# Kernel tuning notes

Measured on AMD Instinct MI355X. Metric: run time of the kernel, lower is better.

## Reference

```python
import jax, jax.numpy as jnp
import numpy as np


def _seg_mean(feat, dst, n):
    # mean aggregation of gathered source features onto destination nodes
    s = jax.ops.segment_sum(feat, dst, num_segments=n)
    c = jax.ops.segment_sum(jnp.ones((dst.shape[0], 1), feat.dtype), dst, num_segments=n)
    return s / jnp.maximum(c, 1.0)


def setup_inputs() -> dict:
    key = jax.random.key(0)
    ks = jax.random.split(key, 16)
    N0, N1, N2 = 400000, 100000, 25000
    E0, E1 = 1600000, 400000
    IN, HID, OUT = 128, 256, 64
    inp = {
        "x_tar": jax.random.normal(ks[0], (N0, IN), jnp.float32),
        "x_neigh": jax.random.normal(ks[1], (N0, IN), jnp.float32),
        "edge_src0": jax.random.randint(ks[2], (E0,), 0, N0, jnp.int64).astype(jnp.int32),
        "edge_dst0": jax.random.randint(ks[3], (E0,), 0, N1, jnp.int64).astype(jnp.int32),
        "edge_src1": jax.random.randint(ks[4], (E1,), 0, N1, jnp.int64).astype(jnp.int32),
        "edge_dst1": jax.random.randint(ks[5], (E1,), 0, N2, jnp.int64).astype(jnp.int32),
        "n_dst0": N1,
        "n_dst1": N2,
    }
    s = 1.0 / np.sqrt(IN)
    sh = 1.0 / np.sqrt(HID)
    inp["Wl0"] = jax.random.uniform(ks[6], (IN, HID), jnp.float32, -s, s)
    inp["Wr0"] = jax.random.uniform(ks[7], (IN, HID), jnp.float32, -s, s)
    inp["b0"] = jnp.zeros((HID,), jnp.float32)
    inp["Wl1"] = jax.random.uniform(ks[8], (HID, HID), jnp.float32, -sh, sh)
    inp["Wr1"] = jax.random.uniform(ks[9], (HID, HID), jnp.float32, -sh, sh)
    inp["b1"] = jnp.zeros((HID,), jnp.float32)
    inp["Wl2"] = jax.random.uniform(ks[10], (HID, OUT), jnp.float32, -sh, sh)
    inp["Wr2"] = jax.random.uniform(ks[11], (HID, OUT), jnp.float32, -sh, sh)
    inp["b2"] = jnp.zeros((OUT,), jnp.float32)
    return inp


def reference(x_tar, x_neigh, edge_src0, edge_dst0, edge_src1, edge_dst1,
              n_dst0, n_dst1, Wl0, Wr0, b0, Wl1, Wr1, b1, Wl2, Wr2, b2):
    # layer 0: precomputed neighbor aggregation -> lin_l(x_neigh) + lin_r(x_tar)
    x = x_neigh @ Wl0 + x_tar @ Wr0 + b0  # [N0, HID]
    # layer 1: bipartite mean-aggregate SAGEConv + relu (eval mode: dropout is identity)
    x_t = x[:n_dst0]
    aggr = _seg_mean(x[edge_src0], edge_dst0, n_dst0)
    x = jax.nn.relu(aggr @ Wl1 + x_t @ Wr1 + b1)  # [N1, HID]
    # layer 2: final SAGEConv
    x_t = x[:n_dst1]
    aggr = _seg_mean(x[edge_src1], edge_dst1, n_dst1)
    out = aggr @ Wl2 + x_t @ Wr2 + b2  # [N2, OUT]
    return jax.nn.log_softmax(out, axis=-1)
```

## Files before the change

kernel.cpp:

```cpp
#include <hip/hip_runtime.h>
#include <hip/hip_bf16.h>

typedef __bf16 bf16_t;
typedef __bf16 bf16x8_t __attribute__((ext_vector_type(8)));
typedef __bf16 bf16x4_t __attribute__((ext_vector_type(4)));
typedef float  f32x4_t  __attribute__((ext_vector_type(4)));

#define N1_ROWS 100000
#define N2_ROWS 25000
#define DIN  128
#define DHID 256
#define DOUT 64
#define CAP  96

__global__ __launch_bounds__(256) void prep_weights(
    const float* __restrict__ Wl0, const float* __restrict__ Wr0,
    const float* __restrict__ Wl1, const float* __restrict__ Wr1,
    const float* __restrict__ Wl2, const float* __restrict__ Wr2,
    bf16_t* __restrict__ Wl0T, bf16_t* __restrict__ Wr0T,
    bf16_t* __restrict__ Wl1T, bf16_t* __restrict__ Wr1T,
    bf16_t* __restrict__ Wl2T, bf16_t* __restrict__ Wr2T) {
  int b = blockIdx.x;
  const float* W; bf16_t* WT; int K, N, base;
  if      (b < 128) { W = Wl0; WT = Wl0T; K = 128; N = 256; base = 0;   }
  else if (b < 256) { W = Wr0; WT = Wr0T; K = 128; N = 256; base = 128; }
  else if (b < 512) { W = Wl1; WT = Wl1T; K = 256; N = 256; base = 256; }
  else if (b < 768) { W = Wr1; WT = Wr1T; K = 256; N = 256; base = 512; }
  else if (b < 832) { W = Wl2; WT = Wl2T; K = 256; N = 64;  base = 768; }
  else              { W = Wr2; WT = Wr2T; K = 256; N = 64;  base = 832; }
  int gid = (b - base) * 256 + threadIdx.x;
  int n = gid / K, k = gid - n * K;
  WT[gid] = (bf16_t)W[(size_t)k * N + n];
}

template<int NT, bool RELU, bool OUTF32, bool AF32>
__global__ __launch_bounds__(256) void gemm_fast(
    const void* __restrict__ A1v, const void* __restrict__ A2v,
    const bf16_t* __restrict__ W1T, const bf16_t* __restrict__ W2T,
    const float* __restrict__ bias, void* __restrict__ outp,
    int M, int K1, int K2) {
  constexpr int BK = 32;
  constexpr int LDA = 40;
  __shared__ bf16_t sA[64 * LDA];
  const int tid  = threadIdx.x;
  const int wave = tid >> 6, lane = tid & 63;
  const int l15  = lane & 15, quad = lane >> 4;
  const int rowBase = blockIdx.x * 64;
  const int colBase = wave * (NT * 16);
  constexpr int NOUT = NT * 64;

  f32x4_t acc[4][NT];
#pragma unroll
  for (int mt = 0; mt < 4; ++mt)
#pragma unroll
    for (int nt = 0; nt < NT; ++nt) acc[mt][nt] = (f32x4_t){0.f, 0.f, 0.f, 0.f};

  const int sr = tid >> 2;
  const int sc = (tid & 3) * 8;
  int gr = rowBase + sr; if (gr >= M) gr = M - 1;

  for (int half = 0; half < 2; ++half) {
    const void* A = half ? A2v : A1v;
    const bf16_t* WT = half ? W2T : W1T;
    const int K = half ? K2 : K1;
    for (int k0 = 0; k0 < K; k0 += BK) {
      bf16x8_t bf[NT];
#pragma unroll
      for (int nt = 0; nt < NT; ++nt)
        bf[nt] = *(const bf16x8_t*)&WT[(size_t)(colBase + nt * 16 + l15) * K + k0 + quad * 8];
      __syncthreads();
      if (AF32) {
        const float* Af = (const float*)A;
        float4 lo = *(const float4*)&Af[(size_t)gr * K + k0 + sc];
        float4 hi = *(const float4*)&Af[(size_t)gr * K + k0 + sc + 4];
        bf16x8_t v;
        v[0] = (bf16_t)lo.x; v[1] = (bf16_t)lo.y; v[2] = (bf16_t)lo.z; v[3] = (bf16_t)lo.w;
        v[4] = (bf16_t)hi.x; v[5] = (bf16_t)hi.y; v[6] = (bf16_t)hi.z; v[7] = (bf16_t)hi.w;
        *(bf16x8_t*)&sA[sr * LDA + sc] = v;
      } else {
        *(uint4*)&sA[sr * LDA + sc] =
            *(const uint4*)&((const bf16_t*)A)[(size_t)gr * K + k0 + sc];
      }
      __syncthreads();
#pragma unroll
      for (int mt = 0; mt < 4; ++mt) {
        bf16x8_t af = *(const bf16x8_t*)&sA[(mt * 16 + l15) * LDA + quad * 8];
#pragma unroll
        for (int nt = 0; nt < NT; ++nt)
          acc[mt][nt] = __builtin_amdgcn_mfma_f32_16x16x32_bf16(af, bf[nt], acc[mt][nt], 0, 0, 0);
      }
    }
  }

  const int rb = rowBase + quad * 4;
#pragma unroll
  for (int mt = 0; mt < 4; ++mt)
#pragma unroll
    for (int nt = 0; nt < NT; ++nt) {
      int col = colBase + nt * 16 + l15;
      float bv = bias[col];
#pragma unroll
      for (int i = 0; i < 4; ++i) {
        int row = rb + mt * 16 + i;
        if (row < M) {
          float v = acc[mt][nt][i] + bv;
          if (RELU) v = fmaxf(v, 0.f);
          if (OUTF32) ((float*)outp)[(size_t)row * NOUT + col] = v;
          else        ((bf16_t*)outp)[(size_t)row * NOUT + col] = (bf16_t)v;
        }
      }
    }
}

__global__ __launch_bounds__(256) void csr_append2(
    const int* __restrict__ s0, const int* __restrict__ d0, int E0,
    int* __restrict__ cnt0, int* __restrict__ csr0,
    const int* __restrict__ s1, const int* __restrict__ d1, int E1,
    int* __restrict__ cnt1, int* __restrict__ csr1, int B0) {
  int b = blockIdx.x;
  if (b < B0) {
    int e = b * 256 + threadIdx.x;
    if (e < E0) {
      int d = d0[e];
      int pos = atomicAdd(&cnt0[d], 1);
      if (pos < CAP) csr0[(size_t)d * CAP + pos] = s0[e];
    }
  } else {
    int e = (b - B0) * 256 + threadIdx.x;
    if (e < E1) {
      int d = d1[e];
      int pos = atomicAdd(&cnt1[d], 1);
      if (pos < CAP) csr1[(size_t)d * CAP + pos] = s1[e];
    }
  }
}

__global__ __launch_bounds__(256) void gather_mean(
    const bf16_t* __restrict__ X, const int* __restrict__ csr,
    const int* __restrict__ cnt, bf16_t* __restrict__ outp, int n) {
  int gid = blockIdx.x * 256 + threadIdx.x;
  int d = gid >> 6, lane = gid & 63;
  if (d >= n) return;
  int deg = cnt[d]; if (deg > CAP) deg = CAP;
  const int* bucket = csr + (size_t)d * CAP;
  f32x4_t A0 = {0,0,0,0}, A1 = {0,0,0,0}, A2 = {0,0,0,0}, A3 = {0,0,0,0};
  int i = 0;
  for (; i + 4 <= deg; i += 4) {
    int s0 = bucket[i], s1 = bucket[i+1], s2 = bucket[i+2], s3 = bucket[i+3];
    bf16x4_t v0 = *(const bf16x4_t*)(X + (size_t)s0 * DHID + lane * 4);
    bf16x4_t v1 = *(const bf16x4_t*)(X + (size_t)s1 * DHID + lane * 4);
    bf16x4_t v2 = *(const bf16x4_t*)(X + (size_t)s2 * DHID + lane * 4);
    bf16x4_t v3 = *(const bf16x4_t*)(X + (size_t)s3 * DHID + lane * 4);
#pragma unroll
    for (int j = 0; j < 4; ++j) {
      A0[j] += (float)v0[j]; A1[j] += (float)v1[j];
      A2[j] += (float)v2[j]; A3[j] += (float)v3[j];
    }
  }
  for (; i < deg; ++i) {
    int s = bucket[i];
    bf16x4_t v = *(const bf16x4_t*)(X + (size_t)s * DHID + lane * 4);
#pragma unroll
    for (int j = 0; j < 4; ++j) A0[j] += (float)v[j];
  }
  float inv = 1.f / (float)(deg > 0 ? deg : 1);
  bf16x4_t o;
#pragma unroll
  for (int j = 0; j < 4; ++j)
    o[j] = (bf16_t)((A0[j] + A1[j] + A2[j] + A3[j]) * inv);
  *(bf16x4_t*)(outp + (size_t)d * DHID + lane * 4) = o;
}

__global__ __launch_bounds__(256) void log_softmax64(
    float* __restrict__ logits, int R) {
  int gid = blockIdx.x * 256 + threadIdx.x;
  int row = gid >> 6, lane = gid & 63;
  if (row >= R) return;
  float v = logits[(size_t)row * DOUT + lane];
  float m = v;
  for (int o = 32; o > 0; o >>= 1) m = fmaxf(m, __shfl_xor(m, o, 64));
  float e = expf(v - m);
  float s = e;
  for (int o = 32; o > 0; o >>= 1) s += __shfl_xor(s, o, 64);
  logits[(size_t)row * DOUT + lane] = v - m - logf(s);
}

extern "C" void kernel_launch(void* const* d_in, const int* in_sizes, int n_in,
                              void* d_out, int out_size, void* d_ws, size_t ws_size,
                              hipStream_t stream) {
  const float* x_tar   = (const float*)d_in[0];
  const float* x_neigh = (const float*)d_in[1];
  const int* es0 = (const int*)d_in[2];
  const int* ed0 = (const int*)d_in[3];
  const int* es1 = (const int*)d_in[4];
  const int* ed1 = (const int*)d_in[5];
  const float* Wl0 = (const float*)d_in[8];
  const float* Wr0 = (const float*)d_in[9];
  const float* b0  = (const float*)d_in[10];
  const float* Wl1 = (const float*)d_in[11];
  const float* Wr1 = (const float*)d_in[12];
  const float* b1  = (const float*)d_in[13];
  const float* Wl2 = (const float*)d_in[14];
  const float* Wr2 = (const float*)d_in[15];
  const float* b2  = (const float*)d_in[16];

  const int E0 = in_sizes[2];
  const int E1 = in_sizes[4];
  const int M0 = in_sizes[0] / DIN;

  char* ws = (char*)d_ws;
  bf16_t* Wl0T = (bf16_t*)(ws + 0);
  bf16_t* Wr0T = (bf16_t*)(ws + 65536);
  bf16_t* Wl1T = (bf16_t*)(ws + 131072);
  bf16_t* Wr1T = (bf16_t*)(ws + 262144);
  bf16_t* Wl2T = (bf16_t*)(ws + 393216);
  bf16_t* Wr2T = (bf16_t*)(ws + 425984);
  bf16_t* x0     = (bf16_t*)(ws + 524288);
  bf16_t* x1     = (bf16_t*)(ws + 524288 + 51200000);
  bf16_t* aggrB  = (bf16_t*)(ws + 205324288);
  bf16_t* aggr2B = (bf16_t*)(ws + 256524288);
  int*    csr0   = (int*)(ws + 269324288);
  int*    csr1   = (int*)(ws + 307724288);
  int*    cnt0   = (int*)(ws + 317324288);
  int*    cnt1   = (int*)(ws + 317724288);
  float*  logits = (float*)d_out;

  prep_weights<<<896, 256, 0, stream>>>(Wl0, Wr0, Wl1, Wr1, Wl2, Wr2,
                                        Wl0T, Wr0T, Wl1T, Wr1T, Wl2T, Wr2T);

  hipMemsetAsync(cnt0, 0, (size_t)(N1_ROWS + N2_ROWS) * 4, stream);

  {
    int B0 = (E0 + 255) / 256, B1 = (E1 + 255) / 256;
    csr_append2<<<B0 + B1, 256, 0, stream>>>(es0, ed0, E0, cnt0, csr0,
                                             es1, ed1, E1, cnt1, csr1, B0);
  }

  gemm_fast<4, false, false, true><<<(M0 + 63) / 64, 256, 0, stream>>>(
      x_neigh, x_tar, Wl0T, Wr0T, b0, x0, M0, DIN, DIN);

  gather_mean<<<(int)(((long long)N1_ROWS * 64 + 255) / 256), 256, 0, stream>>>(
      x0, csr0, cnt0, aggrB, N1_ROWS);

  gemm_fast<4, true, false, false><<<(N1_ROWS + 63) / 64, 256, 0, stream>>>(
      aggrB, x0, Wl1T, Wr1T, b1, x1, N1_ROWS, DHID, DHID);

  gather_mean<<<(int)(((long long)N2_ROWS * 64 + 255) / 256), 256, 0, stream>>>(
      x1, csr1, cnt1, aggr2B, N2_ROWS);

  gemm_fast<1, false, true, false><<<(N2_ROWS + 63) / 64, 256, 0, stream>>>(
      aggr2B, x1, Wl2T, Wr2T, b2, logits, N2_ROWS, DHID, DHID);

  log_softmax64<<<(int)(((long long)N2_ROWS * 64 + 255) / 256), 256, 0, stream>>>(
      logits, N2_ROWS);
}
```

Measured before the change: 942.3 us.

## Stage full-K A tile in LDS once per GEMM half instead of per-32 chunk

The GEMM now loads the whole K extent of each 64-row A tile into shared memory in one pass. For the 128+128 layer both inputs go into one buffer; for the 256-wide layers each input is staged in its own phase. This removes the two barriers per 32-wide K step, issues all global loads up front for more memory-level parallelism, and makes K compile-time constant so loops fully unroll. In exchange LDS use grows to about 33 KB per block, which may reduce occupancy, and the loads are no longer interleaved with MFMA work.

```diff
diff --git a/kernel.cpp b/kernel.cpp
--- a/kernel.cpp
+++ b/kernel.cpp
@@ -33,14 +33,48 @@
   WT[gid] = (bf16_t)W[(size_t)k * N + n];
 }
 
-template<int NT, bool RELU, bool OUTF32, bool AF32>
+template<int KC, int LDA, bool AF32>
+__device__ __forceinline__ void stage_tile(
+    const void* __restrict__ Av, bf16_t* __restrict__ sAp,
+    int gr, int sr, int sc, int colOff) {
+  constexpr int NCH = KC / 32;
+  if (AF32) {
+    const float* Af = (const float*)Av;
+    float4 lo[NCH], hi[NCH];
+#pragma unroll
+    for (int c = 0; c < NCH; ++c) {
+      lo[c] = *(const float4*)&Af[(size_t)gr * KC + sc + c * 32];
+      hi[c] = *(const float4*)&Af[(size_t)gr * KC + sc + c * 32 + 4];
+    }
+#pragma unroll
+    for (int c = 0; c < NCH; ++c) {
+      bf16x8_t v;
+      v[0] = (bf16_t)lo[c].x; v[1] = (bf16_t)lo[c].y;
+      v[2] = (bf16_t)lo[c].z; v[3] = (bf16_t)lo[c].w;
+      v[4] = (bf16_t)hi[c].x; v[5] = (bf16_t)hi[c].y;
+      v[6] = (bf16_t)hi[c].z; v[7] = (bf16_t)hi[c].w;
+      *(bf16x8_t*)&sAp[sr * LDA + colOff + sc + c * 32] = v;
+    }
+  } else {
+    const bf16_t* Ab = (const bf16_t*)Av;
+    uint4 v[NCH];
+#pragma unroll
+    for (int c = 0; c < NCH; ++c)
+      v[c] = *(const uint4*)&Ab[(size_t)gr * KC + sc + c * 32];
+#pragma unroll
+    for (int c = 0; c < NCH; ++c)
+      *(uint4*)&sAp[sr * LDA + colOff + sc + c * 32] = v[c];
+  }
+}
+
+template<int NT, int K1, int K2, bool RELU, bool OUTF32, bool AF32>
 __global__ __launch_bounds__(256) void gemm_fast(
     const void* __restrict__ A1v, const void* __restrict__ A2v,
     const bf16_t* __restrict__ W1T, const bf16_t* __restrict__ W2T,
-    const float* __restrict__ bias, void* __restrict__ outp,
-    int M, int K1, int K2) {
-  constexpr int BK = 32;
-  constexpr int LDA = 40;
+    const float* __restrict__ bias, void* __restrict__ outp, int M) {
+  constexpr bool ONE = (K1 + K2 <= 256);
+  constexpr int KS   = ONE ? (K1 + K2) : (K1 > K2 ? K1 : K2);
+  constexpr int LDA  = KS + 8;
   __shared__ bf16_t sA[64 * LDA];
   const int tid  = threadIdx.x;
   const int wave = tid >> 6, lane = tid & 63;
@@ -59,35 +93,54 @@
   const int sc = (tid & 3) * 8;
   int gr = rowBase + sr; if (gr >= M) gr = M - 1;
 
-  for (int half = 0; half < 2; ++half) {
-    const void* A = half ? A2v : A1v;
-    const bf16_t* WT = half ? W2T : W1T;
-    const int K = half ? K2 : K1;
-    for (int k0 = 0; k0 < K; k0 += BK) {
+  if constexpr (ONE) {
+    stage_tile<K1, LDA, AF32>(A1v, sA, gr, sr, sc, 0);
+    stage_tile<K2, LDA, AF32>(A2v, sA, gr, sr, sc, K1);
+    __syncthreads();
+#pragma unroll
+    for (int ks = 0; ks < (K1 + K2) / 32; ++ks) {
+      const bool h2 = (ks * 32 >= K1);
+      const bf16_t* __restrict__ WT = h2 ? W2T : W1T;
+      const int K  = h2 ? K2 : K1;
+      const int kk = h2 ? (ks * 32 - K1) : (ks * 32);
       bf16x8_t bf[NT];
 #pragma unroll
       for (int nt = 0; nt < NT; ++nt)
-        bf[nt] = *(const bf16x8_t*)&WT[(size_t)(colBase + nt * 16 + l15) * K + k0 + quad * 8];
+        bf[nt] = *(const bf16x8_t*)&WT[(size_t)(colBase + nt * 16 + l15) * K + kk + quad * 8];
+      bf16x8_t af[4];
+#pragma unroll
+      for (int mt = 0; mt < 4; ++mt)
+        af[mt] = *(const bf16x8_t*)&sA[(mt * 16 + l15) * LDA + ks * 32 + quad * 8];
+#pragma unroll
+      for (int mt = 0; mt < 4; ++mt)
+#pragma unroll
+        for (int nt = 0; nt < NT; ++nt)
+          acc[mt][nt] = __builtin_amdgcn_mfma_f32_16x16x32_bf16(af[mt], bf[nt], acc[mt][nt], 0, 0, 0);
+    }
+  } else {
+    static_assert(ONE || K1 == K2, "two-phase path assumes equal K");
+#pragma unroll
+    for (int half = 0; half < 2; ++half) {
+      const bf16_t* __restrict__ WT = half ? W2T : W1T;
+      if (half) __syncthreads();
+      stage_tile<K1, LDA, AF32>(half ? A2v : A1v, sA, gr, sr, sc, 0);
       __syncthreads();
-      if (AF32) {
-        const float* Af = (const float*)A;
-        float4 lo = *(const float4*)&Af[(size_t)gr * K + k0 + sc];
-        float4 hi = *(const float4*)&Af[(size_t)gr * K + k0 + sc + 4];
-        bf16x8_t v;
-        v[0] = (bf16_t)lo.x; v[1] = (bf16_t)lo.y; v[2] = (bf16_t)lo.z; v[3] = (bf16_t)lo.w;
-        v[4] = (bf16_t)hi.x; v[5] = (bf16_t)hi.y; v[6] = (bf16_t)hi.z; v[7] = (bf16_t)hi.w;
-        *(bf16x8_t*)&sA[sr * LDA + sc] = v;
-      } else {
-        *(uint4*)&sA[sr * LDA + sc] =
-            *(const uint4*)&((const bf16_t*)A)[(size_t)gr * K + k0 + sc];
-      }
-      __syncthreads();
-#pragma unroll
-      for (int mt = 0; mt < 4; ++mt) {
-        bf16x8_t af = *(const bf16x8_t*)&sA[(mt * 16 + l15) * LDA + quad * 8];
+#pragma unroll
+      for (int ks = 0; ks < K1 / 32; ++ks) {
+        const int kk = ks * 32;
+        bf16x8_t bf[NT];
 #pragma unroll
         for (int nt = 0; nt < NT; ++nt)
-          acc[mt][nt] = __builtin_amdgcn_mfma_f32_16x16x32_bf16(af, bf[nt], acc[mt][nt], 0, 0, 0);
+          bf[nt] = *(const bf16x8_t*)&WT[(size_t)(colBase + nt * 16 + l15) * K1 + kk + quad * 8];
+        bf16x8_t af[4];
+#pragma unroll
+        for (int mt = 0; mt < 4; ++mt)
+          af[mt] = *(const bf16x8_t*)&sA[(mt * 16 + l15) * LDA + kk + quad * 8];
+#pragma unroll
+        for (int mt = 0; mt < 4; ++mt)
+#pragma unroll
+          for (int nt = 0; nt < NT; ++nt)
+            acc[mt][nt] = __builtin_amdgcn_mfma_f32_16x16x32_bf16(af[mt], bf[nt], acc[mt][nt], 0, 0, 0);
       }
     }
   }
@@ -236,20 +289,20 @@
                                              es1, ed1, E1, cnt1, csr1, B0);
   }
 
-  gemm_fast<4, false, false, true><<<(M0 + 63) / 64, 256, 0, stream>>>(
-      x_neigh, x_tar, Wl0T, Wr0T, b0, x0, M0, DIN, DIN);
+  gemm_fast<4, 128, 128, false, false, true><<<(M0 + 63) / 64, 256, 0, stream>>>(
+      x_neigh, x_tar, Wl0T, Wr0T, b0, x0, M0);
 
   gather_mean<<<(int)(((long long)N1_ROWS * 64 + 255) / 256), 256, 0, stream>>>(
       x0, csr0, cnt0, aggrB, N1_ROWS);
 
-  gemm_fast<4, true, false, false><<<(N1_ROWS + 63) / 64, 256, 0, stream>>>(
-      aggrB, x0, Wl1T, Wr1T, b1, x1, N1_ROWS, DHID, DHID);
+  gemm_fast<4, 256, 256, true, false, false><<<(N1_ROWS + 63) / 64, 256, 0, stream>>>(
+      aggrB, x0, Wl1T, Wr1T, b1, x1, N1_ROWS);
 
   gather_mean<<<(int)(((long long)N2_ROWS * 64 + 255) / 256), 256, 0, stream>>>(
       x1, csr1, cnt1, aggr2B, N2_ROWS);
 
-  gemm_fast<1, false, true, false><<<(N2_ROWS + 63) / 64, 256, 0, stream>>>(
-      aggr2B, x1, Wl2T, Wr2T, b2, logits, N2_ROWS, DHID, DHID);
+  gemm_fast<1, 256, 256, false, true, false><<<(N2_ROWS + 63) / 64, 256, 0, stream>>>(
+      aggr2B, x1, Wl2T, Wr2T, b2, logits, N2_ROWS);
 
   log_softmax64<<<(int)(((long long)N2_ROWS * 64 + 255) / 256), 256, 0, stream>>>(
       logits, N2_ROWS);
```

Measured after the change: 955.8 us. No clear change (+1.4%).
